# Performance work log

Hardware: AMD Instinct MI355X
Metric: run time of the kernel (lower is better)

The kernel has to match this reference:

```python
import jax, jax.numpy as jnp
import numpy as np

N, D_IN, D_OUT = 8192, 1024, 1024

def setup_inputs() -> dict:
    key = jax.random.key(0)
    kx, kq, kk, kv = jax.random.split(key, 4)
    # Linear weights stored as [in_dim, out_dim] (torch stores [out,in]; we pre-transpose)
    s = 1.0 / np.sqrt(D_IN)
    return {
        "x": jax.random.normal(kx, (N, D_IN), dtype=jnp.float32),
        "Wq": jax.random.uniform(kq, (D_IN, D_OUT), dtype=jnp.float32, minval=-s, maxval=s),
        "Wk": jax.random.uniform(kk, (D_IN, D_OUT), dtype=jnp.float32, minval=-s, maxval=s),
        "Wv": jax.random.uniform(kv, (D_IN, D_OUT), dtype=jnp.float32, minval=-s, maxval=s),
    }

def reference(x, Wq, Wk, Wv):
    # Faithful to source: query_w = keys_L(x), key_w = queries_L(x) -- a name swap
    # that is just a relabeling of independent random weights. The earlier
    # parameter matmuls in the source are dead code (overwritten) and omitted.
    q = x @ Wk          # [N, D_OUT]
    k = x @ Wq          # [N, D_OUT]
    v = x @ Wv          # [N, D_OUT]
    scores = (q @ k.T) / jnp.sqrt(jnp.asarray(D_OUT, dtype=q.dtype))  # [N, N]
    weights = jax.nn.softmax(scores, axis=-1)
    return weights @ v  # [N, D_OUT]
```

## Files before the change

### kernel.cpp

```cpp
#include <hip/hip_runtime.h>
#include <hip/hip_bf16.h>
#include <stdint.h>

typedef __bf16 v8bf __attribute__((ext_vector_type(8)));
typedef __bf16 v4bf __attribute__((ext_vector_type(4)));
typedef float  v4f  __attribute__((ext_vector_type(4)));

#define AS1 __attribute__((address_space(1)))
#define AS3 __attribute__((address_space(3)))

__device__ __forceinline__ void load16_lds(const void* g, void* l) {
  __builtin_amdgcn_global_load_lds((const AS1 uint32_t*)g, (AS3 uint32_t*)l, 16, 0, 0);
}

__global__ __launch_bounds__(256) void k_cvt_x(const float* __restrict__ x,
                                               __bf16* __restrict__ xb) {
  size_t i = ((size_t)blockIdx.x * 256 + threadIdx.x) * 4;
  float4 f = *(const float4*)(x + i);
  v4bf b; b[0] = (__bf16)f.x; b[1] = (__bf16)f.y; b[2] = (__bf16)f.z; b[3] = (__bf16)f.w;
  *(v4bf*)(xb + i) = b;
}

__global__ __launch_bounds__(256) void k_wtrans(const float* __restrict__ W,
                                                __bf16* __restrict__ Wt) {
  __shared__ float tile[64][65];
  int r0 = blockIdx.x * 64, c0 = blockIdx.y * 64;
  int t = threadIdx.x;
  #pragma unroll
  for (int p = 0; p < 16; p++) {
    int idx = p * 256 + t; int rr = idx >> 6, cc = idx & 63;
    tile[rr][cc] = W[(size_t)(r0 + rr) * 1024 + c0 + cc];
  }
  __syncthreads();
  #pragma unroll
  for (int p = 0; p < 16; p++) {
    int idx = p * 256 + t; int rr = idx >> 6, cc = idx & 63;
    Wt[(size_t)(c0 + rr) * 1024 + r0 + cc] = (__bf16)tile[cc][rr];
  }
}

__global__ __launch_bounds__(256) void k_vtrans(const __bf16* __restrict__ V,
                                                __bf16* __restrict__ Vt) {
  __shared__ __bf16 tile[64][66];
  int r0 = blockIdx.x * 64, c0 = blockIdx.y * 64;
  int t = threadIdx.x;
  #pragma unroll
  for (int p = 0; p < 16; p++) {
    int idx = p * 256 + t; int rr = idx >> 6, cc = idx & 63;
    tile[rr][cc] = V[(size_t)(r0 + rr) * 1024 + c0 + cc];
  }
  __syncthreads();
  #pragma unroll
  for (int p = 0; p < 16; p++) {
    int idx = p * 256 + t; int rr = idx >> 6, cc = idx & 63;
    Vt[(size_t)(c0 + rr) * 8192 + r0 + cc] = tile[cc][rr];
  }
}

__global__ __launch_bounds__(256) void k_zero(float* __restrict__ p) {
  size_t i = ((size_t)blockIdx.x * 256 + threadIdx.x) * 4;
  *(float4*)(p + i) = make_float4(0.f, 0.f, 0.f, 0.f);
}

__global__ __launch_bounds__(256) void k_rowinv(const float* __restrict__ rs,
                                                float* __restrict__ ri) {
  int i = blockIdx.x * 256 + threadIdx.x;
  ri[i] = 1.0f / rs[i];
}

template <int EPI>
__global__ __launch_bounds__(256, 2) void gemm_nt(
    const __bf16* __restrict__ A, const __bf16* __restrict__ B,
    void* __restrict__ Cout, int M, int N, int K,
    __bf16* __restrict__ qp, __bf16* __restrict__ kp, __bf16* __restrict__ vp,
    float* __restrict__ rowsum, const float* __restrict__ rinv)
{
  __shared__ __bf16 Asm[128 * 64];
  __shared__ __bf16 Bsm[128 * 64];
  const int tid = threadIdx.x;
  const int wave = tid >> 6, lane = tid & 63;
  const size_t m0 = (size_t)blockIdx.x * 128;
  const size_t n0 = (size_t)blockIdx.y * 128;
  const int wm = (wave >> 1) * 64, wn = (wave & 1) * 64;

  v4f acc[4][4];
  #pragma unroll
  for (int i = 0; i < 4; i++)
    #pragma unroll
    for (int j = 0; j < 4; j++) acc[i][j] = (v4f)0.f;

  const int srow8   = lane >> 3;
  const int sgchunk = (lane & 7) ^ srow8;
  const int fr  = lane & 15;
  const int hi  = lane >> 4;
  const int flo = lane & 7;
  const size_t sK = (size_t)K;

  for (int k0 = 0; k0 < K; k0 += 64) {
    #pragma unroll
    for (int p = 0; p < 4; p++) {
      const int seg = p * 4 + wave;
      const int row = seg * 8 + srow8;
      load16_lds(A + (m0 + row) * sK + (size_t)k0 + sgchunk * 8, Asm + seg * 512);
      load16_lds(B + (n0 + row) * sK + (size_t)k0 + sgchunk * 8, Bsm + seg * 512);
    }
    __syncthreads();
    #pragma unroll
    for (int h = 0; h < 2; h++) {
      const int slot = ((h << 2) | hi) ^ flo;
      v8bf a_frag[4], b_frag[4];
      #pragma unroll
      for (int i = 0; i < 4; i++)
        a_frag[i] = *(const v8bf*)(Asm + (wm + i * 16 + fr) * 64 + slot * 8);
      #pragma unroll
      for (int j = 0; j < 4; j++)
        b_frag[j] = *(const v8bf*)(Bsm + (wn + j * 16 + fr) * 64 + slot * 8);
      #pragma unroll
      for (int i = 0; i < 4; i++)
        #pragma unroll
        for (int j = 0; j < 4; j++)
          acc[i][j] = __builtin_amdgcn_mfma_f32_16x16x32_bf16(a_frag[i], b_frag[j], acc[i][j], 0, 0, 0);
    }
    __syncthreads();
  }

  const int er = (lane >> 4) * 4;
  const int ec = lane & 15;

  if (EPI == 3) {
    float rpart[4][4];
    #pragma unroll
    for (int i = 0; i < 4; i++)
      #pragma unroll
      for (int r = 0; r < 4; r++) rpart[i][r] = 0.f;
    #pragma unroll
    for (int i = 0; i < 4; i++)
      #pragma unroll
      for (int j = 0; j < 4; j++) {
        const size_t col = n0 + wn + j * 16 + ec;
        #pragma unroll
        for (int r = 0; r < 4; r++) {
          const size_t rowg = m0 + wm + i * 16 + er + r;
          float e = __expf(acc[i][j][r]);
          ((__bf16*)Cout)[rowg * (size_t)N + col] = (__bf16)e;
          rpart[i][r] += e;
        }
      }
    #pragma unroll
    for (int i = 0; i < 4; i++)
      #pragma unroll
      for (int r = 0; r < 4; r++) {
        float s = rpart[i][r];
        s += __shfl_xor(s, 1); s += __shfl_xor(s, 2);
        s += __shfl_xor(s, 4); s += __shfl_xor(s, 8);
        if (ec == 0) atomicAdd(&rowsum[m0 + wm + i * 16 + er + r], s);
      }
    return;
  }

  #pragma unroll
  for (int i = 0; i < 4; i++)
    #pragma unroll
    for (int j = 0; j < 4; j++) {
      const size_t col = n0 + wn + j * 16 + ec;
      #pragma unroll
      for (int r = 0; r < 4; r++) {
        const size_t rowg = m0 + wm + i * 16 + er + r;
        float val = acc[i][j][r];
        if (EPI == 0) {
          ((float*)Cout)[rowg * (size_t)N + col] = val * rinv[rowg];
        } else {
          const int buf = (int)(col >> 10);
          const size_t cc = col & 1023;
          __bf16* dst = (buf == 0) ? qp : ((buf == 1) ? kp : vp);
          if (buf == 0) val *= 0.03125f;
          dst[rowg * 1024 + cc] = (__bf16)val;
        }
      }
    }
}

extern "C" void kernel_launch(void* const* d_in, const int* in_sizes, int n_in,
                              void* d_out, int out_size, void* d_ws, size_t ws_size,
                              hipStream_t stream) {
  const float* x  = (const float*)d_in[0];
  const float* Wq = (const float*)d_in[1];
  const float* Wk = (const float*)d_in[2];
  const float* Wv = (const float*)d_in[3];
  float* out = (float*)d_out;

  const size_t N = 8192, D = 1024;
  char* ws = (char*)d_ws;
  size_t off = 0;
  __bf16* xb = (__bf16*)(ws + off); off += N * D * 2;
  __bf16* wt = (__bf16*)(ws + off); off += 3 * D * D * 2;
  __bf16* q  = (__bf16*)(ws + off); off += N * D * 2;
  __bf16* k  = (__bf16*)(ws + off); off += N * D * 2;
  __bf16* v  = (__bf16*)(ws + off); off += N * D * 2;
  __bf16* vt = (__bf16*)(ws + off); off += N * D * 2;
  __bf16* S  = (__bf16*)(ws + off); off += N * N * 2;
  float* rowsum = (float*)(ws + off); off += N * 4;
  float* rinv   = (float*)(ws + off); off += N * 4;
  if (ws_size < off) return;

  k_cvt_x<<<dim3(8192), dim3(256), 0, stream>>>(x, xb);
  k_wtrans<<<dim3(16, 16), dim3(256), 0, stream>>>(Wk, wt);
  k_wtrans<<<dim3(16, 16), dim3(256), 0, stream>>>(Wq, wt + D * D);
  k_wtrans<<<dim3(16, 16), dim3(256), 0, stream>>>(Wv, wt + 2 * D * D);
  k_zero<<<dim3(8), dim3(256), 0, stream>>>(rowsum);
  gemm_nt<2><<<dim3(64, 24), dim3(256), 0, stream>>>(xb, wt, nullptr, 8192, 3072, 1024, q, k, v, nullptr, nullptr);
  k_vtrans<<<dim3(128, 16), dim3(256), 0, stream>>>(v, vt);
  gemm_nt<3><<<dim3(64, 64), dim3(256), 0, stream>>>(q, k, S, 8192, 8192, 1024, nullptr, nullptr, nullptr, rowsum, nullptr);
  k_rowinv<<<dim3(32), dim3(256), 0, stream>>>(rowsum, rinv);
  gemm_nt<0><<<dim3(64, 8), dim3(256), 0, stream>>>(S, vt, out, 8192, 1024, 8192, nullptr, nullptr, nullptr, nullptr, rinv);
}
```

Measured before the change: 426.8 us.

## Use 256x256 double-buffered pipelined GEMM with split-K for PV product

Replaces the 128x128 single-buffered GEMM with a 256x256 tile, 8-wave kernel. It double-buffers LDS, interleaves global-to-LDS prefetch with MFMA phases, and uses setprio and barriers to schedule the work. The final S·V GEMM is split along K into two partial fp32 buffers, which a new combine kernel sums and normalizes by the row sums. The aim is more data reuse per tile and hiding load latency behind compute, at the cost of extra fp32 partial traffic, larger LDS use, and reusing the workspace start (the xb/wt region) for the partials.

After: 468.4 us. 9.7% more time.

```diff
diff --git a/kernel.cpp b/kernel.cpp
--- a/kernel.cpp
+++ b/kernel.cpp
@@ -62,79 +62,173 @@
   *(float4*)(p + i) = make_float4(0.f, 0.f, 0.f, 0.f);
 }
 
-__global__ __launch_bounds__(256) void k_rowinv(const float* __restrict__ rs,
-                                                float* __restrict__ ri) {
-  int i = blockIdx.x * 256 + threadIdx.x;
-  ri[i] = 1.0f / rs[i];
+__global__ __launch_bounds__(256) void k_combine(const float* __restrict__ p0,
+                                                 const float* __restrict__ p1,
+                                                 const float* __restrict__ rowsum,
+                                                 float* __restrict__ out) {
+  size_t i = ((size_t)blockIdx.x * 256 + threadIdx.x) * 4;
+  float4 a = *(const float4*)(p0 + i);
+  float4 b = *(const float4*)(p1 + i);
+  float ri = 1.0f / rowsum[i >> 10];
+  float4 o;
+  o.x = (a.x + b.x) * ri; o.y = (a.y + b.y) * ri;
+  o.z = (a.z + b.z) * ri; o.w = (a.w + b.w) * ri;
+  *(float4*)(out + i) = o;
 }
 
 template <int EPI>
-__global__ __launch_bounds__(256, 2) void gemm_nt(
+__global__ __launch_bounds__(512, 2) void gemm256(
     const __bf16* __restrict__ A, const __bf16* __restrict__ B,
-    void* __restrict__ Cout, int M, int N, int K,
+    void* __restrict__ Cout, int M, int N, int KS, int lda, int ldb,
     __bf16* __restrict__ qp, __bf16* __restrict__ kp, __bf16* __restrict__ vp,
-    float* __restrict__ rowsum, const float* __restrict__ rinv)
+    float* __restrict__ rowsum)
 {
-  __shared__ __bf16 Asm[128 * 64];
-  __shared__ __bf16 Bsm[128 * 64];
-  const int tid = threadIdx.x;
+  __shared__ __bf16 Asm[2][256 * 64];
+  __shared__ __bf16 Bsm[2][256 * 64];
+
+  const int tid  = threadIdx.x;
   const int wave = tid >> 6, lane = tid & 63;
-  const size_t m0 = (size_t)blockIdx.x * 128;
-  const size_t n0 = (size_t)blockIdx.y * 128;
-  const int wm = (wave >> 1) * 64, wn = (wave & 1) * 64;
-
-  v4f acc[4][4];
-  #pragma unroll
-  for (int i = 0; i < 4; i++)
-    #pragma unroll
-    for (int j = 0; j < 4; j++) acc[i][j] = (v4f)0.f;
+  const int wm = (wave >> 2) * 128;
+  const int wn = (wave & 3) * 64;
+  const size_t m0 = (size_t)blockIdx.x * 256;
+  const size_t n0 = (size_t)blockIdx.y * 256;
+  const int NT = KS >> 6;
+  const int kz = blockIdx.z * KS;
 
   const int srow8   = lane >> 3;
   const int sgchunk = (lane & 7) ^ srow8;
   const int fr  = lane & 15;
   const int hi  = lane >> 4;
   const int flo = lane & 7;
-  const size_t sK = (size_t)K;
-
-  for (int k0 = 0; k0 < K; k0 += 64) {
-    #pragma unroll
-    for (int p = 0; p < 4; p++) {
-      const int seg = p * 4 + wave;
-      const int row = seg * 8 + srow8;
-      load16_lds(A + (m0 + row) * sK + (size_t)k0 + sgchunk * 8, Asm + seg * 512);
-      load16_lds(B + (n0 + row) * sK + (size_t)k0 + sgchunk * 8, Bsm + seg * 512);
-    }
-    __syncthreads();
-    #pragma unroll
-    for (int h = 0; h < 2; h++) {
-      const int slot = ((h << 2) | hi) ^ flo;
-      v8bf a_frag[4], b_frag[4];
+
+  const size_t slda = (size_t)lda, sldb = (size_t)ldb;
+
+  v4f acc[8][4];
+  #pragma unroll
+  for (int i = 0; i < 8; i++)
+    #pragma unroll
+    for (int j = 0; j < 4; j++) acc[i][j] = (v4f)0.f;
+
+  auto stageA = [&](int v, int R0) {
+    const int kk = kz + (v < NT ? v : NT - 1) * 64;
+    const __bf16* s = A + (m0 + R0 + wave * 8 + srow8) * slda + kk + sgchunk * 8;
+    __bf16* d = &Asm[v & 1][(R0 + wave * 8) * 64];
+    load16_lds(s, d);
+    load16_lds(s + 64 * slda, d + 64 * 64);
+  };
+  auto stageB = [&](int v, int R0) {
+    const int kk = kz + (v < NT ? v : NT - 1) * 64;
+    const __bf16* s = B + (n0 + R0 + wave * 8 + srow8) * sldb + kk + sgchunk * 8;
+    __bf16* d = &Bsm[v & 1][(R0 + wave * 8) * 64];
+    load16_lds(s, d);
+    load16_lds(s + 64 * sldb, d + 64 * 64);
+  };
+
+  stageA(0, 0); stageA(0, 128);
+  stageB(0, 0); stageB(0, 128);
+  stageB(1, 0); stageB(1, 128);
+  asm volatile("s_waitcnt vmcnt(4)" ::: "memory");
+  __builtin_amdgcn_s_barrier();
+
+  v8bf aq[4][2], bA[2][2], bB[2][2];
+
+  for (int t = 0; t < NT; t++) {
+    const int c = t & 1;
+    const __bf16* Ab = Asm[c];
+    const __bf16* Bb = Bsm[c];
+
+    #pragma unroll
+    for (int i = 0; i < 4; i++)
+      #pragma unroll
+      for (int h = 0; h < 2; h++)
+        aq[i][h] = *(const v8bf*)(Ab + (wm + i * 16 + fr) * 64 + ((((h << 2) | hi) ^ flo) * 8));
+    #pragma unroll
+    for (int j = 0; j < 2; j++)
+      #pragma unroll
+      for (int h = 0; h < 2; h++)
+        bA[j][h] = *(const v8bf*)(Bb + (wn + j * 16 + fr) * 64 + ((((h << 2) | hi) ^ flo) * 8));
+    stageA(t + 1, 0);
+    __builtin_amdgcn_s_barrier();
+    asm volatile("s_waitcnt lgkmcnt(0)" ::: "memory");
+    __builtin_amdgcn_sched_barrier(0);
+    __builtin_amdgcn_s_setprio(1);
+    #pragma unroll
+    for (int h = 0; h < 2; h++)
       #pragma unroll
       for (int i = 0; i < 4; i++)
-        a_frag[i] = *(const v8bf*)(Asm + (wm + i * 16 + fr) * 64 + slot * 8);
-      #pragma unroll
-      for (int j = 0; j < 4; j++)
-        b_frag[j] = *(const v8bf*)(Bsm + (wn + j * 16 + fr) * 64 + slot * 8);
+        #pragma unroll
+        for (int j = 0; j < 2; j++)
+          acc[i][j] = __builtin_amdgcn_mfma_f32_16x16x32_bf16(aq[i][h], bA[j][h], acc[i][j], 0, 0, 0);
+    __builtin_amdgcn_s_setprio(0);
+    __builtin_amdgcn_s_barrier();
+
+    #pragma unroll
+    for (int j = 0; j < 2; j++)
+      #pragma unroll
+      for (int h = 0; h < 2; h++)
+        bB[j][h] = *(const v8bf*)(Bb + (wn + (j + 2) * 16 + fr) * 64 + ((((h << 2) | hi) ^ flo) * 8));
+    stageA(t + 1, 128);
+    __builtin_amdgcn_s_barrier();
+    asm volatile("s_waitcnt lgkmcnt(0)" ::: "memory");
+    __builtin_amdgcn_sched_barrier(0);
+    __builtin_amdgcn_s_setprio(1);
+    #pragma unroll
+    for (int h = 0; h < 2; h++)
       #pragma unroll
       for (int i = 0; i < 4; i++)
         #pragma unroll
-        for (int j = 0; j < 4; j++)
-          acc[i][j] = __builtin_amdgcn_mfma_f32_16x16x32_bf16(a_frag[i], b_frag[j], acc[i][j], 0, 0, 0);
-    }
-    __syncthreads();
+        for (int j = 0; j < 2; j++)
+          acc[i][j + 2] = __builtin_amdgcn_mfma_f32_16x16x32_bf16(aq[i][h], bB[j][h], acc[i][j + 2], 0, 0, 0);
+    __builtin_amdgcn_s_setprio(0);
+    __builtin_amdgcn_s_barrier();
+
+    #pragma unroll
+    for (int i = 0; i < 4; i++)
+      #pragma unroll
+      for (int h = 0; h < 2; h++)
+        aq[i][h] = *(const v8bf*)(Ab + (wm + (i + 4) * 16 + fr) * 64 + ((((h << 2) | hi) ^ flo) * 8));
+    stageB(t + 2, 0);
+    __builtin_amdgcn_s_barrier();
+    asm volatile("s_waitcnt lgkmcnt(0)" ::: "memory");
+    __builtin_amdgcn_sched_barrier(0);
+    __builtin_amdgcn_s_setprio(1);
+    #pragma unroll
+    for (int h = 0; h < 2; h++)
+      #pragma unroll
+      for (int i = 0; i < 4; i++)
+        #pragma unroll
+        for (int j = 0; j < 2; j++)
+          acc[i + 4][j + 2] = __builtin_amdgcn_mfma_f32_16x16x32_bf16(aq[i][h], bB[j][h], acc[i + 4][j + 2], 0, 0, 0);
+    __builtin_amdgcn_s_setprio(0);
+    __builtin_amdgcn_s_barrier();
+
+    stageB(t + 2, 128);
+    __builtin_amdgcn_s_barrier();
+    __builtin_amdgcn_sched_barrier(0);
+    __builtin_amdgcn_s_setprio(1);
+    #pragma unroll
+    for (int h = 0; h < 2; h++)
+      #pragma unroll
+      for (int i = 0; i < 4; i++)
+        #pragma unroll
+        for (int j = 0; j < 2; j++)
+          acc[i + 4][j] = __builtin_amdgcn_mfma_f32_16x16x32_bf16(aq[i][h], bA[j][h], acc[i + 4][j], 0, 0, 0);
+    __builtin_amdgcn_s_setprio(0);
+    asm volatile("s_waitcnt vmcnt(4)" ::: "memory");
+    __builtin_amdgcn_s_barrier();
   }
 
   const int er = (lane >> 4) * 4;
   const int ec = lane & 15;
 
   if (EPI == 3) {
-    float rpart[4][4];
-    #pragma unroll
-    for (int i = 0; i < 4; i++)
+    float rpart[8][4];
+    #pragma unroll
+    for (int i = 0; i < 8; i++)
       #pragma unroll
       for (int r = 0; r < 4; r++) rpart[i][r] = 0.f;
     #pragma unroll
-    for (int i = 0; i < 4; i++)
+    for (int i = 0; i < 8; i++)
       #pragma unroll
       for (int j = 0; j < 4; j++) {
         const size_t col = n0 + wn + j * 16 + ec;
@@ -147,7 +241,7 @@
         }
       }
     #pragma unroll
-    for (int i = 0; i < 4; i++)
+    for (int i = 0; i < 8; i++)
       #pragma unroll
       for (int r = 0; r < 4; r++) {
         float s = rpart[i][r];
@@ -159,7 +253,7 @@
   }
 
   #pragma unroll
-  for (int i = 0; i < 4; i++)
+  for (int i = 0; i < 8; i++)
     #pragma unroll
     for (int j = 0; j < 4; j++) {
       const size_t col = n0 + wn + j * 16 + ec;
@@ -167,8 +261,9 @@
       for (int r = 0; r < 4; r++) {
         const size_t rowg = m0 + wm + i * 16 + er + r;
         float val = acc[i][j][r];
-        if (EPI == 0) {
-          ((float*)Cout)[rowg * (size_t)N + col] = val * rinv[rowg];
+        if (EPI == 1) {
+          float* po = (float*)Cout + (size_t)blockIdx.z * ((size_t)M * (size_t)N);
+          po[rowg * (size_t)N + col] = val;
         } else {
           const int buf = (int)(col >> 10);
           const size_t cc = col & 1023;
@@ -200,7 +295,7 @@
   __bf16* vt = (__bf16*)(ws + off); off += N * D * 2;
   __bf16* S  = (__bf16*)(ws + off); off += N * N * 2;
   float* rowsum = (float*)(ws + off); off += N * 4;
-  float* rinv   = (float*)(ws + off); off += N * 4;
+  float* pp = (float*)ws;
   if (ws_size < off) return;
 
   k_cvt_x<<<dim3(8192), dim3(256), 0, stream>>>(x, xb);
@@ -208,9 +303,9 @@
   k_wtrans<<<dim3(16, 16), dim3(256), 0, stream>>>(Wq, wt + D * D);
   k_wtrans<<<dim3(16, 16), dim3(256), 0, stream>>>(Wv, wt + 2 * D * D);
   k_zero<<<dim3(8), dim3(256), 0, stream>>>(rowsum);
-  gemm_nt<2><<<dim3(64, 24), dim3(256), 0, stream>>>(xb, wt, nullptr, 8192, 3072, 1024, q, k, v, nullptr, nullptr);
+  gemm256<2><<<dim3(32, 12), dim3(512), 0, stream>>>(xb, wt, nullptr, 8192, 3072, 1024, 1024, 1024, q, k, v, nullptr);
   k_vtrans<<<dim3(128, 16), dim3(256), 0, stream>>>(v, vt);
-  gemm_nt<3><<<dim3(64, 64), dim3(256), 0, stream>>>(q, k, S, 8192, 8192, 1024, nullptr, nullptr, nullptr, rowsum, nullptr);
-  k_rowinv<<<dim3(32), dim3(256), 0, stream>>>(rowsum, rinv);
-  gemm_nt<0><<<dim3(64, 8), dim3(256), 0, stream>>>(S, vt, out, 8192, 1024, 8192, nullptr, nullptr, nullptr, nullptr, rinv);
-}
+  gemm256<3><<<dim3(32, 32), dim3(512), 0, stream>>>(q, k, S, 8192, 8192, 1024, 1024, 1024, nullptr, nullptr, nullptr, rowsum);
+  gemm256<1><<<dim3(32, 4, 2), dim3(512), 0, stream>>>(S, vt, pp, 8192, 1024, 4096, 8192, 8192, nullptr, nullptr, nullptr, nullptr);
+  k_combine<<<dim3(8192), dim3(256), 0, stream>>>(pp, pp + N * D, rowsum, out);
+}
```
